# Performance work log

Hardware: AMD Instinct MI355X
Metric: run time of the kernel (lower is better)

Reference implementation:

```python
import jax, jax.numpy as jnp
import numpy as np


def setup_inputs() -> dict:
    key = jax.random.key(0)
    B, H, N = 1024, 8, 64
    A = jax.random.normal(key, (B, H, N, N), dtype=jnp.float32)
    # Build SPD matrices: P = A A^T / N + eps * I (eigenvalues strictly > 0)
    P = jnp.einsum('bhij,bhkj->bhik', A, A) / N + 1e-3 * jnp.eye(N, dtype=jnp.float32)
    return {"P": P}


def reference(P):
    # LogEig: eigendecompose each SPD matrix, take log of eigenvalues,
    # reconstruct X = U diag(log w) U^T  (batched over [B, H]).
    w, U = jnp.linalg.eigh(P)          # w: [B,H,N], U: [B,H,N,N]
    logw = jnp.log(w)
    return jnp.einsum('bhik,bhk,bhjk->bhij', U, logw, U)
```

## Files before the change

kernel.cpp:

```cpp
#include <hip/hip_runtime.h>
#include <math.h>

#define N 64
#define LDC 68
#define MAX_SWEEPS 10
#define SKIP_TOL2 9e-12f

__device__ __forceinline__ float frcp(float x)   { return __builtin_amdgcn_rcpf(x); }
__device__ __forceinline__ float fsqrt_(float x) { return __builtin_amdgcn_sqrtf(x); }
__device__ __forceinline__ float frsq(float x)   { return __builtin_amdgcn_rsqf(x); }
__device__ __forceinline__ float flog_(float x)  { return __builtin_amdgcn_logf(x) * 0.69314718056f; }

__device__ __forceinline__ float bperm(int idx, float v) {
    return __int_as_float(__builtin_amdgcn_ds_bpermute(idx, __float_as_int(v)));
}

__global__ __launch_bounds__(64, 2)
void logeig_kernel(const float* __restrict__ P, float* __restrict__ Out) {
    __shared__ float As[N * LDC];
    __shared__ float lw_s[N];

    const int t = threadIdx.x;
    const int bid = blockIdx.x;
    const float* A0 = P + (size_t)bid * (N * N);
    float* O = Out + (size_t)bid * (N * N);

    {
        const float4* A4 = (const float4*)A0;
        #pragma unroll
        for (int kk = 0; kk < 16; ++kk) {
            int f = kk * 64 + t;
            float4 v = A4[f];
            int e = f << 2;
            int r = e >> 6;
            int i = e & 63;
            *(float4*)&As[r * LDC + i] = v;
        }
    }
    __syncthreads();

    for (int k = 0; k < N; ++k) {
        float dval = fmaxf(As[k * LDC + k], 1e-20f);
        float dinv = frsq(dval);
        {
            int i = k + 1 + t;
            if (i < N) As[k * LDC + i] *= dinv;
        }
        if (t == 0) As[k * LDC + k] = dval * dinv;
        __syncthreads();
        for (int j = k + 1 + (t >> 3); j < N; j += 8) {
            float ljk = As[k * LDC + j];
            for (int i = j + (t & 7); i < N; i += 8)
                As[j * LDC + i] = fmaf(-As[k * LDC + i], ljk, As[j * LDC + i]);
        }
        __syncthreads();
    }

    for (int f = t; f < N * N; f += 64) {
        int cc = f >> 6, i = f & 63;
        if (i < cc) As[cc * LDC + i] = 0.f;
    }
    __syncthreads();

    float own[N];
    #pragma unroll
    for (int i4 = 0; i4 < 16; ++i4) {
        float4 v = *(const float4*)&As[t * LDC + 4 * i4];
        own[4 * i4 + 0] = v.x;
        own[4 * i4 + 1] = v.y;
        own[4 * i4 + 2] = v.z;
        own[4 * i4 + 3] = v.w;
    }
    float nrm;
    {
        float d0 = 0.f, d1 = 0.f, d2 = 0.f, d3 = 0.f;
        #pragma unroll
        for (int i = 0; i < N; i += 4) {
            d0 = fmaf(own[i + 0], own[i + 0], d0);
            d1 = fmaf(own[i + 1], own[i + 1], d1);
            d2 = fmaf(own[i + 2], own[i + 2], d2);
            d3 = fmaf(own[i + 3], own[i + 3], d3);
        }
        nrm = (d0 + d1) + (d2 + d3);
    }

    int conv = 0;
    #pragma unroll 1
    for (int sweep = 0; sweep < MAX_SWEEPS && !conv; ++sweep) {
        int rot = 0;
        #pragma unroll 1
        for (int r = 0; r < 63; ++r) {
            int pl;
            bool top;
            if (t == 63)     { pl = r;  top = true;  }
            else if (t == r) { pl = 63; top = false; }
            else {
                pl = 2 * r - t;
                if (pl < 0) pl += 63; else if (pl >= 63) pl -= 63;
                int d = t - r; if (d < 0) d += 63;
                top = (d <= 31);
            }
            int idx = pl << 2;
            float bn = bperm(idx, nrm);
            float prt[N];
            #pragma unroll
            for (int i = 0; i < N; ++i) prt[i] = bperm(idx, own[i]);
            float d0 = 0.f, d1 = 0.f, d2 = 0.f, d3 = 0.f;
            #pragma unroll
            for (int i = 0; i < N; i += 4) {
                d0 = fmaf(own[i + 0], prt[i + 0], d0);
                d1 = fmaf(own[i + 1], prt[i + 1], d1);
                d2 = fmaf(own[i + 2], prt[i + 2], d2);
                d3 = fmaf(own[i + 3], prt[i + 3], d3);
            }
            float gd = (d0 + d1) + (d2 + d3);
            float a = top ? nrm : bn;
            float b = top ? bn : nrm;
            if (gd * gd > SKIP_TOL2 * a * b) {
                float tau = (b - a) * 0.5f * frcp(gd);
                float tt = frcp(fabsf(tau) + fsqrt_(fmaf(tau, tau, 1.f)));
                if (tau < 0.f) tt = -tt;
                float c = frsq(fmaf(tt, tt, 1.f));
                float s = tt * c;
                float sg = top ? -s : s;
                #pragma unroll
                for (int i = 0; i < N; ++i)
                    own[i] = fmaf(sg, prt[i], c * own[i]);
                float tsg = top ? -tt : tt;
                nrm = fmaf(tsg, gd, nrm);
                rot = 1;
            }
        }
        conv = !__any(rot);
    }

    #pragma unroll
    for (int i4 = 0; i4 < 16; ++i4) {
        float4 v = make_float4(own[4 * i4 + 0], own[4 * i4 + 1],
                               own[4 * i4 + 2], own[4 * i4 + 3]);
        *(float4*)&As[t * LDC + 4 * i4] = v;
    }
    {
        float d0 = 0.f, d1 = 0.f, d2 = 0.f, d3 = 0.f;
        #pragma unroll
        for (int i = 0; i < N; i += 4) {
            d0 = fmaf(own[i + 0], own[i + 0], d0);
            d1 = fmaf(own[i + 1], own[i + 1], d1);
            d2 = fmaf(own[i + 2], own[i + 2], d2);
            d3 = fmaf(own[i + 3], own[i + 3], d3);
        }
        float lam = fmaxf((d0 + d1) + (d2 + d3), 1e-30f);
        lw_s[t] = flog_(lam) * frcp(lam);
    }
    __syncthreads();

    {
        int ti = t >> 4;
        int tj = t & 15;
        float acc[16][4];
        #pragma unroll
        for (int a2 = 0; a2 < 16; ++a2)
            #pragma unroll
            for (int b2 = 0; b2 < 4; ++b2) acc[a2][b2] = 0.f;

        for (int k = 0; k < N; ++k) {
            float w = lw_s[k];
            const float* ck = &As[k * LDC];
            float4 ub = *(const float4*)&ck[4 * tj];
            ub.x *= w; ub.y *= w; ub.z *= w; ub.w *= w;
            float vb[4] = {ub.x, ub.y, ub.z, ub.w};
            float4 ua0 = *(const float4*)&ck[16 * ti + 0];
            float4 ua1 = *(const float4*)&ck[16 * ti + 4];
            float4 ua2 = *(const float4*)&ck[16 * ti + 8];
            float4 ua3 = *(const float4*)&ck[16 * ti + 12];
            float va[16] = {ua0.x, ua0.y, ua0.z, ua0.w,
                            ua1.x, ua1.y, ua1.z, ua1.w,
                            ua2.x, ua2.y, ua2.z, ua2.w,
                            ua3.x, ua3.y, ua3.z, ua3.w};
            #pragma unroll
            for (int a2 = 0; a2 < 16; ++a2)
                #pragma unroll
                for (int b2 = 0; b2 < 4; ++b2)
                    acc[a2][b2] = fmaf(va[a2], vb[b2], acc[a2][b2]);
        }
        #pragma unroll
        for (int a2 = 0; a2 < 16; ++a2) {
            float4 vout = make_float4(acc[a2][0], acc[a2][1], acc[a2][2], acc[a2][3]);
            ((float4*)O)[(16 * ti + a2) * 16 + tj] = vout;
        }
    }
}

extern "C" void kernel_launch(void* const* d_in, const int* in_sizes, int n_in,
                              void* d_out, int out_size, void* d_ws, size_t ws_size,
                              hipStream_t stream) {
    const float* P = (const float*)d_in[0];
    float* Out = (float*)d_out;
    int nmat = in_sizes[0] / (N * N);
    logeig_kernel<<<dim3(nmat), dim3(64), 0, stream>>>(P, Out);
}
```

Before: 3.504 ms.

## Transpose Jacobi layout so lanes hold rows and rotations use register shifts

Switches the one-sided Jacobi sweep from one column per lane, which needed 64 ds_bpermute exchanges per round, to each lane holding one row with column pairs kept in adjacent registers. Dot products are now built by a cross-lane reduction tree using permlane32/16 swaps and ds_swizzle. Rotation coefficients are broadcast with readlane, and the round-robin pairing is done by shifting registers, with one bpermute for the norms. This removes most LDS permute traffic but adds many readlane operations and always-executed rotations, and it relies on gfx950-specific permlane swap instructions.

Result: no change. 3.517 ms (+0.4%).

```diff
diff --git a/kernel.cpp b/kernel.cpp
--- a/kernel.cpp
+++ b/kernel.cpp
@@ -11,8 +11,25 @@
 __device__ __forceinline__ float frsq(float x)   { return __builtin_amdgcn_rsqf(x); }
 __device__ __forceinline__ float flog_(float x)  { return __builtin_amdgcn_logf(x) * 0.69314718056f; }
 
-__device__ __forceinline__ float bperm(int idx, float v) {
-    return __int_as_float(__builtin_amdgcn_ds_bpermute(idx, __float_as_int(v)));
+template <int IMM>
+__device__ __forceinline__ float swz(float x) {
+    return __int_as_float(__builtin_amdgcn_ds_swizzle(__float_as_int(x), IMM));
+}
+template <int CTRL>
+__device__ __forceinline__ float dppmov(float x) {
+    return __int_as_float(__builtin_amdgcn_update_dpp(0, __float_as_int(x), CTRL, 0xF, 0xF, true));
+}
+__device__ __forceinline__ void pl32_swap(float& a, float& b) {
+    asm volatile("v_permlane32_swap_b32 %0, %1" : "+v"(a), "+v"(b));
+}
+__device__ __forceinline__ void pl16_swap(float& a, float& b) {
+    asm volatile("v_permlane16_swap_b32 %0, %1" : "+v"(a), "+v"(b));
+}
+__device__ __forceinline__ float bperm(int byteidx, float v) {
+    return __int_as_float(__builtin_amdgcn_ds_bpermute(byteidx, __float_as_int(v)));
+}
+__device__ __forceinline__ float rdlane(float v, int lane) {
+    return __int_as_float(__builtin_amdgcn_readlane(__float_as_int(v), lane));
 }
 
 __global__ __launch_bounds__(64, 2)
@@ -62,92 +79,128 @@
     }
     __syncthreads();
 
-    float own[N];
+    float R[N];
     #pragma unroll
-    for (int i4 = 0; i4 < 16; ++i4) {
-        float4 v = *(const float4*)&As[t * LDC + 4 * i4];
-        own[4 * i4 + 0] = v.x;
-        own[4 * i4 + 1] = v.y;
-        own[4 * i4 + 2] = v.z;
-        own[4 * i4 + 3] = v.w;
-    }
+    for (int c2 = 0; c2 < N; ++c2) R[c2] = As[c2 * LDC + t];
+
     float nrm;
     {
         float d0 = 0.f, d1 = 0.f, d2 = 0.f, d3 = 0.f;
-        #pragma unroll
-        for (int i = 0; i < N; i += 4) {
-            d0 = fmaf(own[i + 0], own[i + 0], d0);
-            d1 = fmaf(own[i + 1], own[i + 1], d1);
-            d2 = fmaf(own[i + 2], own[i + 2], d2);
-            d3 = fmaf(own[i + 3], own[i + 3], d3);
+        const float* cc = &As[t * LDC];
+        #pragma unroll
+        for (int j = 0; j < 16; ++j) {
+            float4 v = *(const float4*)&cc[4 * j];
+            d0 = fmaf(v.x, v.x, d0);
+            d1 = fmaf(v.y, v.y, d1);
+            d2 = fmaf(v.z, v.z, d2);
+            d3 = fmaf(v.w, v.w, d3);
         }
         nrm = (d0 + d1) + (d2 + d3);
     }
 
-    int conv = 0;
+    int bidx;
+    {
+        int pl;
+        if (t == 0) pl = 0;
+        else if (t == 2) pl = 1;
+        else if ((t & 1) == 0) pl = t - 2;
+        else if (t == 63) pl = 62;
+        else pl = t + 2;
+        bidx = pl << 2;
+    }
+
+    const bool m8 = (t & 8) != 0, m4 = (t & 4) != 0, m2 = (t & 2) != 0;
+    const bool ev = (t & 1) == 0;
+
     #pragma unroll 1
-    for (int sweep = 0; sweep < MAX_SWEEPS && !conv; ++sweep) {
-        int rot = 0;
+    for (int sweep = 0; sweep < MAX_SWEEPS; ++sweep) {
+        int rs = 0;
         #pragma unroll 1
         for (int r = 0; r < 63; ++r) {
-            int pl;
-            bool top;
-            if (t == 63)     { pl = r;  top = true;  }
-            else if (t == r) { pl = 63; top = false; }
-            else {
-                pl = 2 * r - t;
-                if (pl < 0) pl += 63; else if (pl >= 63) pl -= 63;
-                int d = t - r; if (d < 0) d += 63;
-                top = (d <= 31);
-            }
-            int idx = pl << 2;
-            float bn = bperm(idx, nrm);
-            float prt[N];
-            #pragma unroll
-            for (int i = 0; i < N; ++i) prt[i] = bperm(idx, own[i]);
-            float d0 = 0.f, d1 = 0.f, d2 = 0.f, d3 = 0.f;
-            #pragma unroll
-            for (int i = 0; i < N; i += 4) {
-                d0 = fmaf(own[i + 0], prt[i + 0], d0);
-                d1 = fmaf(own[i + 1], prt[i + 1], d1);
-                d2 = fmaf(own[i + 2], prt[i + 2], d2);
-                d3 = fmaf(own[i + 3], prt[i + 3], d3);
-            }
-            float gd = (d0 + d1) + (d2 + d3);
-            float a = top ? nrm : bn;
-            float b = top ? bn : nrm;
-            if (gd * gd > SKIP_TOL2 * a * b) {
-                float tau = (b - a) * 0.5f * frcp(gd);
-                float tt = frcp(fabsf(tau) + fsqrt_(fmaf(tau, tau, 1.f)));
-                if (tau < 0.f) tt = -tt;
-                float c = frsq(fmaf(tt, tt, 1.f));
-                float s = tt * c;
-                float sg = top ? -s : s;
+            float Pr[32];
+            #pragma unroll
+            for (int v = 0; v < 32; ++v) Pr[v] = R[2 * v] * R[2 * v + 1];
+            #pragma unroll
+            for (int v = 0; v < 16; ++v) {
+                float a = Pr[v], b = Pr[v + 16];
+                pl32_swap(a, b);
+                Pr[v] = a + b;
+            }
+            #pragma unroll
+            for (int v = 0; v < 8; ++v) {
+                float a = Pr[v], b = Pr[v + 8];
+                pl16_swap(a, b);
+                Pr[v] = a + b;
+            }
+            #pragma unroll
+            for (int v = 0; v < 4; ++v) {
+                float f0 = Pr[v] + swz<0x201F>(Pr[v]);
+                float f1 = Pr[v + 4] + swz<0x201F>(Pr[v + 4]);
+                Pr[v] = m8 ? f1 : f0;
+            }
+            #pragma unroll
+            for (int v = 0; v < 2; ++v) {
+                float f0 = Pr[v] + swz<0x101F>(Pr[v]);
+                float f1 = Pr[v + 2] + swz<0x101F>(Pr[v + 2]);
+                Pr[v] = m4 ? f1 : f0;
+            }
+            {
+                float f0 = Pr[0] + swz<0x081F>(Pr[0]);
+                float f1 = Pr[1] + swz<0x081F>(Pr[1]);
+                Pr[0] = m2 ? f1 : f0;
+            }
+            float gd = Pr[0] + swz<0x041F>(Pr[0]);
+
+            float other = dppmov<0xB1>(nrm);
+            float a = ev ? nrm : other;
+            float b = ev ? other : nrm;
+            bool dorot = (gd * gd > SKIP_TOL2 * a * b);
+            float tau = (b - a) * 0.5f * frcp(gd);
+            float tt = frcp(fabsf(tau) + fsqrt_(fmaf(tau, tau, 1.f)));
+            if (tau < 0.f) tt = -tt;
+            tt = dorot ? tt : 0.f;
+            float c = dorot ? frsq(fmaf(tt, tt, 1.f)) : 1.f;
+            float s = dorot ? tt * c : 0.f;
+            nrm = fmaf(ev ? -tt : tt, gd, nrm);
+            rs |= (int)dorot;
+
+            #pragma unroll
+            for (int j = 0; j < 32; ++j) {
+                float cj = rdlane(c, 2 * j);
+                float sj = rdlane(s, 2 * j);
+                float t0 = R[2 * j], t1 = R[2 * j + 1];
+                R[2 * j]     = cj * t0 - sj * t1;
+                R[2 * j + 1] = sj * t0 + cj * t1;
+            }
+
+            {
+                float tX31 = R[62], tY0 = R[1];
                 #pragma unroll
-                for (int i = 0; i < N; ++i)
-                    own[i] = fmaf(sg, prt[i], c * own[i]);
-                float tsg = top ? -tt : tt;
-                nrm = fmaf(tsg, gd, nrm);
-                rot = 1;
-            }
-        }
-        conv = !__any(rot);
+                for (int j = 31; j >= 2; --j) R[2 * j] = R[2 * j - 2];
+                R[2] = tY0;
+                #pragma unroll
+                for (int j = 0; j <= 30; ++j) R[2 * j + 1] = R[2 * j + 3];
+                R[63] = tX31;
+                nrm = bperm(bidx, nrm);
+            }
+        }
+        if (!__any(rs)) break;
     }
 
     #pragma unroll
-    for (int i4 = 0; i4 < 16; ++i4) {
-        float4 v = make_float4(own[4 * i4 + 0], own[4 * i4 + 1],
-                               own[4 * i4 + 2], own[4 * i4 + 3]);
-        *(float4*)&As[t * LDC + 4 * i4] = v;
-    }
+    for (int c2 = 0; c2 < N; ++c2) As[c2 * LDC + t] = R[c2];
+    __syncthreads();
+
     {
         float d0 = 0.f, d1 = 0.f, d2 = 0.f, d3 = 0.f;
-        #pragma unroll
-        for (int i = 0; i < N; i += 4) {
-            d0 = fmaf(own[i + 0], own[i + 0], d0);
-            d1 = fmaf(own[i + 1], own[i + 1], d1);
-            d2 = fmaf(own[i + 2], own[i + 2], d2);
-            d3 = fmaf(own[i + 3], own[i + 3], d3);
+        const float* cc = &As[t * LDC];
+        #pragma unroll
+        for (int j = 0; j < 16; ++j) {
+            float4 v = *(const float4*)&cc[4 * j];
+            d0 = fmaf(v.x, v.x, d0);
+            d1 = fmaf(v.y, v.y, d1);
+            d2 = fmaf(v.z, v.z, d2);
+            d3 = fmaf(v.w, v.w, d3);
         }
         float lam = fmaxf((d0 + d1) + (d2 + d3), 1e-30f);
         lw_s[t] = flog_(lam) * frcp(lam);
```
